# Kernel optimization log

Measured on AMD Instinct MI355X. Metric: run time of the kernel, lower is better.

The kernel has to match this reference:

```python
import jax, jax.numpy as jnp
import numpy as np

THRESH = 0.5
DECAY = 0.2
N_NODES = 39
T = 2000
K_HOPS = 3


def setup_inputs() -> dict:
    key = jax.random.key(0)
    ks = jax.random.split(key, 10)
    x = jax.random.normal(ks[0], (N_NODES, 2, T), dtype=jnp.float32)
    edge_index = jax.random.randint(ks[1], (2, 156), 0, N_NODES)
    # TAGConv(2, 64, K=3): (K+1) bias-free hop weights + single bias
    W_conv = jax.random.normal(ks[2], (K_HOPS + 1, 2, 64), dtype=jnp.float32) * 0.3
    b_conv = jax.random.normal(ks[3], (64,), dtype=jnp.float32) * 0.05
    W1 = jax.random.normal(ks[4], (N_NODES * 64, 128), dtype=jnp.float32) * 0.02
    b1 = jax.random.normal(ks[5], (128,), dtype=jnp.float32) * 0.02
    W2 = jax.random.normal(ks[6], (128, 256), dtype=jnp.float32) * 0.08
    b2 = jax.random.normal(ks[7], (256,), dtype=jnp.float32) * 0.02
    W3 = jax.random.normal(ks[8], (256, 36), dtype=jnp.float32) * 0.06
    b3 = jax.random.normal(ks[9], (36,), dtype=jnp.float32) * 0.02
    return {"x": x, "edge_index": edge_index, "W_conv": W_conv, "b_conv": b_conv,
            "W1": W1, "b1": b1, "W2": W2, "b2": b2, "W3": W3, "b3": b3}


def _norm_adj(edge_index, dtype):
    # PyG gcn_norm without self loops: A_hat = D^-1/2 A D^-1/2, message flows row->col
    row, col = edge_index[0], edge_index[1]
    A = jnp.zeros((N_NODES, N_NODES), dtype).at[col, row].add(1.0)
    deg = A.sum(axis=1)
    dinv = jnp.where(deg > 0, deg ** -0.5, 0.0).astype(dtype)
    return dinv[:, None] * A * dinv[None, :]


def reference(x, edge_index, W_conv, b_conv, W1, b1, W2, b2, W3, b3):
    A_hat = _norm_adj(edge_index, x.dtype)

    def spike(m):
        return (m > THRESH).astype(m.dtype)

    def step(carry, xt):
        c1m, c1s, h1m, h1s, h2m, h2s, h3m, h3s, acc = carry
        # TAGConv: sum_k (A_hat^k xt) @ W_k + bias   [39,64]
        h = xt
        conv = h @ W_conv[0]
        for k in range(1, K_HOPS + 1):
            h = A_hat @ h
            conv = conv + h @ W_conv[k]
        conv = conv + b_conv
        c1m = c1m * DECAY * (1.0 - c1s) + conv
        c1s = spike(c1m)
        f = c1s.reshape(-1)  # [2496]
        h1m = h1m * DECAY * (1.0 - h1s) + f @ W1 + b1
        h1s = spike(h1m)
        h2m = h2m * DECAY * (1.0 - h2s) + h1s @ W2 + b2
        h2s = spike(h2m)
        h3m = h3m * DECAY * (1.0 - h3s) + h2s @ W3 + b3
        h3s = spike(h3m)
        return (c1m, c1s, h1m, h1s, h2m, h2s, h3m, h3s, acc + h3s), None

    z = lambda s: jnp.zeros(s, x.dtype)
    init = (z((N_NODES, 64)), z((N_NODES, 64)), z((128,)), z((128,)),
            z((256,)), z((256,)), z((36,)), z((36,)), z((36,)))
    xs = jnp.moveaxis(x, -1, 0)  # [T, 39, 2]
    carry, _ = jax.lax.scan(step, init, xs)
    return carry[-1] / x.shape[-1]
```

## Files before the change

### kernel.cpp

```cpp
#include <hip/hip_runtime.h>

#define T 2000
#define K1N 2496
#define K2 4992
#define TL 48
#define NCHB 42
#define MAXNZ 24

using short8 = __attribute__((ext_vector_type(8))) short;
using floatx4 = __attribute__((ext_vector_type(4))) float;

__device__ __forceinline__ unsigned bf16_rne(float v) {
    unsigned u = __float_as_uint(v);
    return (u + 0x7FFFu + ((u >> 16) & 1u)) >> 16;
}
__device__ __forceinline__ unsigned packhl(float w) {
    unsigned hi = bf16_rne(w);
    float r = w - __uint_as_float(hi << 16);
    unsigned lo = bf16_rne(r);
    return (hi & 0xFFFFu) | (lo << 16);
}

__global__ __launch_bounds__(256) void conv_scan(const float* __restrict__ x,
        const int* __restrict__ ei, const float* __restrict__ Wc,
        const float* __restrict__ bc, unsigned char* __restrict__ FS,
        const float* __restrict__ W1, unsigned* __restrict__ W1t,
        float* __restrict__ out) {
    __shared__ float ah[1560];
    __shared__ float2 alist[39 * MAXNZ];
    __shared__ int nnzr[40];
    __shared__ float bufA[78 * TL];
    __shared__ float bufB[78 * TL];
    __shared__ float feat[4 * TL * 8];
    int tid = threadIdx.x;
    int nb = blockIdx.x, ch = blockIdx.y;
    int bl = ch * 10 + nb;

    if (bl == 0 && tid < 36) out[tid] = 0.f;

    for (int u = tid; u < 1521; u += 256) ah[u] = 0.f;
    __syncthreads();
    if (tid < 156) atomicAdd(&ah[ei[156 + tid] * 39 + ei[tid]], 1.f);
    __syncthreads();
    if (tid < 39) {
        float d = 0.f;
        for (int u = 0; u < 39; ++u) d += ah[tid * 39 + u];
        ah[1521 + tid] = (d > 0.f) ? (1.f / sqrtf(d)) : 0.f;
    }
    __syncthreads();
    for (int u = tid; u < 1521; u += 256) {
        int i = u / 39, j = u - i * 39;
        ah[u] = (ah[1521 + i] * ah[u]) * ah[1521 + j];
    }
    __syncthreads();
    if (tid < 39) {
        int cnt = 0;
        for (int m = 0; m < 39; ++m) {
            float v = ah[tid * 39 + m];
            if (v != 0.f && cnt < MAXNZ) {
                alist[tid * MAXNZ + cnt] = make_float2(v, __int_as_float((2 * m) * TL * 4));
                ++cnt;
            }
        }
        nnzr[tid] = cnt;
    }
    __syncthreads();

    int t0 = ch * TL;
    int i0 = nb * 4;
    int iloc = tid >> 6, j = tid & 63;
    bool vn = (i0 + iloc) < 39;
    float wv[8], bias;
    #pragma unroll
    for (int q = 0; q < 8; ++q) wv[q] = Wc[q * 64 + j];
    bias = bc[j];
    float m = 0.f, s = 0.f;

    for (int st = 0; st < 2; ++st) {
        int ts = t0 + (st - 1) * TL;
        if (ts < 0) continue;
        for (int e = tid; e < 78 * TL; e += 256) {
            int r = e / TL, tt = e - (e / TL) * TL;
            int t = ts + tt;
            bufA[e] = (t < T) ? x[r * T + t] : 0.f;
        }
        __syncthreads();
        for (int e = tid; e < 384; e += 256) {
            int lr = e / TL, tt = e - (e / TL) * TL;
            int gr = i0 * 2 + lr;
            float v = (gr < 78) ? bufA[gr * TL + tt] : 0.f;
            feat[(((lr >> 1) * TL) + tt) * 8 + (lr & 1)] = v;
        }
        for (int e = tid; e < 468; e += 256) {
            int r = e / 6, g = e - (e / 6) * 6;
            int ii = r >> 1, c = r & 1;
            float acc[8];
            #pragma unroll
            for (int u = 0; u < 8; ++u) acc[u] = 0.f;
            int nz = nnzr[ii];
            const float2* lp = &alist[ii * MAXNZ];
            int cg = c * (TL * 4) + g * 32;
            for (int q = 0; q < nz; ++q) {
                float2 av = lp[q];
                const float* xp = (const float*)((const char*)bufA + (__float_as_int(av.y) + cg));
                float a = av.x;
                float4 x0 = *(const float4*)xp;
                float4 x1 = *(const float4*)(xp + 4);
                acc[0] += a * x0.x; acc[1] += a * x0.y; acc[2] += a * x0.z; acc[3] += a * x0.w;
                acc[4] += a * x1.x; acc[5] += a * x1.y; acc[6] += a * x1.z; acc[7] += a * x1.w;
            }
            float* dp = &bufB[r * TL + g * 8];
            *(float4*)dp = *(float4*)&acc[0];
            *(float4*)(dp + 4) = *(float4*)&acc[4];
        }
        __syncthreads();
        for (int e = tid; e < 384; e += 256) {
            int lr = e / TL, tt = e - (e / TL) * TL;
            int gr = i0 * 2 + lr;
            float v = (gr < 78) ? bufB[gr * TL + tt] : 0.f;
            feat[(((lr >> 1) * TL) + tt) * 8 + 2 + (lr & 1)] = v;
        }
        for (int e = tid; e < 468; e += 256) {
            int r = e / 6, g = e - (e / 6) * 6;
            int ii = r >> 1, c = r & 1;
            float acc[8];
            #pragma unroll
            for (int u = 0; u < 8; ++u) acc[u] = 0.f;
            int nz = nnzr[ii];
            const float2* lp = &alist[ii * MAXNZ];
            int cg = c * (TL * 4) + g * 32;
            for (int q = 0; q < nz; ++q) {
                float2 av = lp[q];
                const float* xp = (const float*)((const char*)bufB + (__float_as_int(av.y) + cg));
                float a = av.x;
                float4 x0 = *(const float4*)xp;
                float4 x1 = *(const float4*)(xp + 4);
                acc[0] += a * x0.x; acc[1] += a * x0.y; acc[2] += a * x0.z; acc[3] += a * x0.w;
                acc[4] += a * x1.x; acc[5] += a * x1.y; acc[6] += a * x1.z; acc[7] += a * x1.w;
            }
            float* dp = &bufA[r * TL + g * 8];
            *(float4*)dp = *(float4*)&acc[0];
            *(float4*)(dp + 4) = *(float4*)&acc[4];
        }
        __syncthreads();
        for (int e = tid; e < 384; e += 256) {
            int lr = e / TL, tt = e - (e / TL) * TL;
            int gr = i0 * 2 + lr;
            float v = (gr < 78) ? bufA[gr * TL + tt] : 0.f;
            feat[(((lr >> 1) * TL) + tt) * 8 + 4 + (lr & 1)] = v;
        }
        for (int e = tid; e < 48; e += 256) {
            int lr = e / 6, g = e - (e / 6) * 6;
            int gi = i0 + (lr >> 1), c = lr & 1, il = lr >> 1;
            float acc[8];
            #pragma unroll
            for (int u = 0; u < 8; ++u) acc[u] = 0.f;
            if (gi < 39) {
                int nz = nnzr[gi];
                const float2* lp = &alist[gi * MAXNZ];
                int cg = c * (TL * 4) + g * 32;
                for (int q = 0; q < nz; ++q) {
                    float2 av = lp[q];
                    const float* xp = (const float*)((const char*)bufA + (__float_as_int(av.y) + cg));
                    float a = av.x;
                    float4 x0 = *(const float4*)xp;
                    float4 x1 = *(const float4*)(xp + 4);
                    acc[0] += a * x0.x; acc[1] += a * x0.y; acc[2] += a * x0.z; acc[3] += a * x0.w;
                    acc[4] += a * x1.x; acc[5] += a * x1.y; acc[6] += a * x1.z; acc[7] += a * x1.w;
                }
            }
            #pragma unroll
            for (int u = 0; u < 8; ++u)
                feat[((il * TL) + g * 8 + u) * 8 + 6 + c] = acc[u];
        }
        __syncthreads();
        for (int tt = 0; tt < TL; ++tt) {
            const float4* fp = (const float4*)&feat[((iloc * TL) + tt) * 8];
            float4 f0 = fp[0], f1 = fp[1];
            float acc = 0.f;
            acc += wv[0] * f0.x; acc += wv[1] * f0.y; acc += wv[2] * f0.z; acc += wv[3] * f0.w;
            acc += wv[4] * f1.x; acc += wv[5] * f1.y; acc += wv[6] * f1.z; acc += wv[7] * f1.w;
            float v = acc + bias;
            m = m * 0.2f * (1.f - s) + v;
            s = (m > 0.5f) ? 1.f : 0.f;
            if (st == 1 && vn) {
                int t = ts + tt;
                if (t < T) FS[t * K1N + (nb * 256 + tid)] = (unsigned char)(s != 0.f);
            }
        }
        __syncthreads();
    }
    const int total = 128 * K1N;
    for (int f = bl * 256 + tid; f < total; f += 420 * 256) {
        int k = f >> 7, jj = f & 127;
        W1t[jj * K1N + k] = packhl(W1[f]);
    }
}

__global__ __launch_bounds__(256) void gemm1(const unsigned char* __restrict__ FS,
        const short* __restrict__ W1t, float* __restrict__ F1p) {
    __shared__ short As[32 * 72];
    __shared__ short Ws[128 * 72];
    int tid = threadIdx.x;
    int t0 = blockIdx.x * 32;
    int ks = blockIdx.y;
    int lane = tid & 63, wvi = tid >> 6;
    int j0 = wvi * 32;
    int row = lane & 15, quad = lane >> 4;
    floatx4 a00 = {0.f, 0.f, 0.f, 0.f};
    floatx4 a01 = a00, a10 = a00, a11 = a00;
    int kb = ks * 416, kb2 = ks * 832;
    int sm = tid >> 3, sb4 = (tid & 7) * 4;
    int gt = t0 + sm;
    int jjv[4], kov[4];
    #pragma unroll
    for (int u = 0; u < 4; ++u) {
        int aid = u * 256 + tid;
        jjv[u] = aid >> 3;
        kov[u] = (aid & 7) * 8;
    }
    unsigned u4 = 0;
    short8 wr0, wr1, wr2, wr3;
    if (gt < T) u4 = *(const unsigned*)&FS[gt * K1N + kb + sb4];
    wr0 = *(const short8*)&W1t[jjv[0] * K2 + kb2 + kov[0]];
    wr1 = *(const short8*)&W1t[jjv[1] * K2 + kb2 + kov[1]];
    wr2 = *(const short8*)&W1t[jjv[2] * K2 + kb2 + kov[2]];
    wr3 = *(const short8*)&W1t[jjv[3] * K2 + kb2 + kov[3]];
    for (int c = 0; c < 13; ++c) {
        uint4 dd;
        dd.x = (u4 & 0x000000FFu) ? 0x3F803F80u : 0u;
        dd.y = (u4 & 0x0000FF00u) ? 0x3F803F80u : 0u;
        dd.z = (u4 & 0x00FF0000u) ? 0x3F803F80u : 0u;
        dd.w = (u4 & 0xFF000000u) ? 0x3F803F80u : 0u;
        *(uint4*)&As[sm * 72 + sb4 * 2] = dd;
        *(short8*)&Ws[jjv[0] * 72 + kov[0]] = wr0;
        *(short8*)&Ws[jjv[1] * 72 + kov[1]] = wr1;
        *(short8*)&Ws[jjv[2] * 72 + kov[2]] = wr2;
        *(short8*)&Ws[jjv[3] * 72 + kov[3]] = wr3;
        __syncthreads();
        unsigned u4n = 0;
        short8 wn0, wn1, wn2, wn3;
        if (c < 12) {
            if (gt < T) u4n = *(const unsigned*)&FS[gt * K1N + kb + (c + 1) * 32 + sb4];
            wn0 = *(const short8*)&W1t[jjv[0] * K2 + kb2 + (c + 1) * 64 + kov[0]];
            wn1 = *(const short8*)&W1t[jjv[1] * K2 + kb2 + (c + 1) * 64 + kov[1]];
            wn2 = *(const short8*)&W1t[jjv[2] * K2 + kb2 + (c + 1) * 64 + kov[2]];
            wn3 = *(const short8*)&W1t[jjv[3] * K2 + kb2 + (c + 1) * 64 + kov[3]];
        }
        #pragma unroll
        for (int sh = 0; sh < 2; ++sh) {
            int k0 = sh * 32 + quad * 8;
            short8 fa0 = *(const short8*)&As[row * 72 + k0];
            short8 fa1 = *(const short8*)&As[(row + 16) * 72 + k0];
            short8 fb0 = *(const short8*)&Ws[(j0 + row) * 72 + k0];
            short8 fb1 = *(const short8*)&Ws[(j0 + 16 + row) * 72 + k0];
            a00 = __builtin_amdgcn_mfma_f32_16x16x32_bf16(fa0, fb0, a00, 0, 0, 0);
            a01 = __builtin_amdgcn_mfma_f32_16x16x32_bf16(fa0, fb1, a01, 0, 0, 0);
            a10 = __builtin_amdgcn_mfma_f32_16x16x32_bf16(fa1, fb0, a10, 0, 0, 0);
            a11 = __builtin_amdgcn_mfma_f32_16x16x32_bf16(fa1, fb1, a11, 0, 0, 0);
        }
        __syncthreads();
        if (c < 12) { u4 = u4n; wr0 = wn0; wr1 = wn1; wr2 = wn2; wr3 = wn3; }
    }
    #pragma unroll
    for (int r = 0; r < 4; ++r) {
        int m0 = quad * 4 + r;
        int t = t0 + m0;
        if (t < T) {
            F1p[t * 768 + ks * 128 + j0 + row] = a00[r];
            F1p[t * 768 + ks * 128 + j0 + 16 + row] = a01[r];
        }
        int t2 = t0 + 16 + m0;
        if (t2 < T) {
            F1p[t2 * 768 + ks * 128 + j0 + row] = a10[r];
            F1p[t2 * 768 + ks * 128 + j0 + 16 + row] = a11[r];
        }
    }
}

__global__ __launch_bounds__(256) void h1_gemm2(const float* __restrict__ F1p,
        const float* __restrict__ b1, const float* __restrict__ W2,
        float* __restrict__ G2) {
    __shared__ float AT[128 * 8];
    int tid = threadIdx.x;
    int t0 = blockIdx.x * 8;
    if (tid < 128) {
        int n = tid;
        int hs = t0 - 20; if (hs < 0) hs = 0;
        float b = b1[n];
        float m = 0.f, s = 0.f;
        for (int tg = hs; tg < t0 + 8; tg += 4) {
            float vb[4][6];
            #pragma unroll
            for (int u = 0; u < 4; ++u)
                #pragma unroll
                for (int q = 0; q < 6; ++q)
                    vb[u][q] = F1p[(tg + u) * 768 + q * 128 + n];
            #pragma unroll
            for (int u = 0; u < 4; ++u) {
                float v = 0.f;
                #pragma unroll
                for (int q = 0; q < 6; ++q) v += vb[u][q];
                v += b;
                m = m * 0.2f * (1.f - s) + v;
                s = (m > 0.5f) ? 1.f : 0.f;
                int t = tg + u;
                if (t >= t0) AT[n * 8 + (t - t0)] = s;
            }
        }
    }
    __syncthreads();
    int j = tid;
    float acc[8] = {0.f};
    #pragma unroll 4
    for (int k = 0; k < 128; ++k) {
        float w = W2[k * 256 + j];
        float4 q0 = *(const float4*)&AT[k * 8 + 0];
        float4 q1 = *(const float4*)&AT[k * 8 + 4];
        acc[0] += q0.x * w; acc[1] += q0.y * w; acc[2] += q0.z * w; acc[3] += q0.w * w;
        acc[4] += q1.x * w; acc[5] += q1.y * w; acc[6] += q1.z * w; acc[7] += q1.w * w;
    }
    #pragma unroll
    for (int tt = 0; tt < 8; ++tt) G2[(t0 + tt) * 256 + j] = acc[tt];
}

__global__ __launch_bounds__(256) void tail(const float* __restrict__ G2,
        const float* __restrict__ b2, const float* __restrict__ W3,
        const float* __restrict__ b3, float* __restrict__ out) {
    __shared__ float w3t[36 * 260];
    __shared__ unsigned char S2[76 * 260];
    __shared__ float G3[76 * 36];
    int tid = threadIdx.x;
    int t0 = blockIdx.x * 25;
    int gs = t0 - 50; if (gs < 0) gs = 0;
    int hs = gs - 50; if (hs < 0) hs = 0;
    int L3 = t0 + 25 - gs;
    #pragma unroll
    for (int u = 0; u < 9; ++u) {
        int f = u * 1024 + tid * 4;
        float4 wq = *(const float4*)&W3[f];
        int k0 = f / 36, j0 = f - k0 * 36;
        float wv[4] = {wq.x, wq.y, wq.z, wq.w};
        #pragma unroll
        for (int q = 0; q < 4; ++q) {
            int k = (j0 + q >= 36) ? k0 + 1 : k0;
            int jj = (j0 + q >= 36) ? (j0 + q - 36) : (j0 + q);
            w3t[jj * 260 + k] = wv[q];
        }
    }
    {
        int n = tid;
        float b = b2[n];
        float m = 0.f, s = 0.f;
        for (int base = hs; base < t0 + 25; base += 25) {
            float vb[25];
            #pragma unroll
            for (int u = 0; u < 25; ++u) vb[u] = G2[(base + u) * 256 + n];
            #pragma unroll
            for (int u = 0; u < 25; ++u) {
                float v = vb[u] + b;
                m = m * 0.2f * (1.f - s) + v;
                s = (m > 0.5f) ? 1.f : 0.f;
                int t = base + u;
                if (t >= gs) S2[(t - gs) * 260 + n] = (unsigned char)(s != 0.f);
            }
        }
    }
    __syncthreads();
    for (int e = tid; e < 36 * 19; e += 256) {
        int jj = e / 19, g = e - (e / 19) * 19;
        int tb = g * 4;
        if (tb >= L3) continue;
        float ac0 = 0.f, ac1 = 0.f, ac2 = 0.f, ac3 = 0.f;
        const unsigned char* r0 = &S2[tb * 260];
        for (int k = 0; k < 256; k += 4) {
            float4 w = *(const float4*)&w3t[jj * 260 + k];
            uchar4 q0 = *(const uchar4*)&r0[k];
            uchar4 q1 = *(const uchar4*)&r0[260 + k];
            uchar4 q2 = *(const uchar4*)&r0[520 + k];
            uchar4 q3 = *(const uchar4*)&r0[780 + k];
            ac0 += (float)q0.x * w.x + (float)q0.y * w.y + (float)q0.z * w.z + (float)q0.w * w.w;
            ac1 += (float)q1.x * w.x + (float)q1.y * w.y + (float)q1.z * w.z + (float)q1.w * w.w;
            ac2 += (float)q2.x * w.x + (float)q2.y * w.y + (float)q2.z * w.z + (float)q2.w * w.w;
            ac3 += (float)q3.x * w.x + (float)q3.y * w.y + (float)q3.z * w.z + (float)q3.w * w.w;
        }
        G3[tb * 36 + jj] = ac0;
        if (tb + 1 < L3) G3[(tb + 1) * 36 + jj] = ac1;
        if (tb + 2 < L3) G3[(tb + 2) * 36 + jj] = ac2;
        if (tb + 3 < L3) G3[(tb + 3) * 36 + jj] = ac3;
    }
    __syncthreads();
    if (tid < 36) {
        int n = tid;
        float b = b3[n];
        float m = 0.f, s = 0.f;
        int cnt = 0;
        for (int t = gs; t < t0 + 25; ++t) {
            float v = G3[(t - gs) * 36 + n] + b;
            m = m * 0.2f * (1.f - s) + v;
            s = (m > 0.5f) ? 1.f : 0.f;
            if (t >= t0) cnt += (s != 0.f) ? 1 : 0;
        }
        atomicAdd(&out[n], (float)cnt * 0.0005f);
    }
}

extern "C" void kernel_launch(void* const* d_in, const int* in_sizes, int n_in,
                              void* d_out, int out_size, void* d_ws, size_t ws_size,
                              hipStream_t stream) {
    const float* x  = (const float*)d_in[0];
    const int*   ei = (const int*)d_in[1];
    const float* Wc = (const float*)d_in[2];
    const float* bc = (const float*)d_in[3];
    const float* W1 = (const float*)d_in[4];
    const float* b1 = (const float*)d_in[5];
    const float* W2 = (const float*)d_in[6];
    const float* b2 = (const float*)d_in[7];
    const float* W3 = (const float*)d_in[8];
    const float* b3 = (const float*)d_in[9];
    float* out = (float*)d_out;

    float* w = (float*)d_ws;
    float* F1p = w;                       w += (size_t)T * 768;
    float* G2  = w;                       w += (size_t)T * 256;
    unsigned* W1t = (unsigned*)w;         w += 128 * K1N;
    unsigned char* FS = (unsigned char*)w;

    conv_scan<<<dim3(10, NCHB), 256, 0, stream>>>(x, ei, Wc, bc, FS, W1, W1t, out);
    gemm1<<<dim3(63, 6), 256, 0, stream>>>(FS, (const short*)W1t, F1p);
    h1_gemm2<<<250, 256, 0, stream>>>(F1p, b1, W2, G2);
    tail<<<80, 256, 0, stream>>>(G2, b2, W3, b3, out);
}
```

Baseline: 161.2 us.

## Fuse h1 scan, MFMA layer-2 GEMM and tail into one windowed kernel

Merges the h1 spike scan, the W2 GEMM, the h2/h3 scans and the W3 product into one kernel. Each block owns 20 output steps and replays a 120-step warm-up window in 32-step tiles, which removes the global G2 round trip and one launch. The 128x256 GEMM now runs on bf16 MFMA using a hi/lo split of W2, prepacked in the conv kernel. In exchange there is redundant warm-up work, since each block recomputes 140 steps. Correctness depends on the spike state converging within the window.

After: 259.0 us. +60.7%, slower.

```diff
diff --git a/kernel.cpp b/kernel.cpp
--- a/kernel.cpp
+++ b/kernel.cpp
@@ -6,6 +6,8 @@
 #define TL 48
 #define NCHB 42
 #define MAXNZ 24
+#define L3 20
+#define NB3 100
 
 using short8 = __attribute__((ext_vector_type(8))) short;
 using floatx4 = __attribute__((ext_vector_type(4))) float;
@@ -25,6 +27,7 @@
         const int* __restrict__ ei, const float* __restrict__ Wc,
         const float* __restrict__ bc, unsigned char* __restrict__ FS,
         const float* __restrict__ W1, unsigned* __restrict__ W1t,
+        const float* __restrict__ W2, unsigned* __restrict__ W2t,
         float* __restrict__ out) {
     __shared__ float ah[1560];
     __shared__ float2 alist[39 * MAXNZ];
@@ -194,6 +197,10 @@
     for (int f = bl * 256 + tid; f < total; f += 420 * 256) {
         int k = f >> 7, jj = f & 127;
         W1t[jj * K1N + k] = packhl(W1[f]);
+    }
+    for (int f = bl * 256 + tid; f < 128 * 256; f += 420 * 256) {
+        int k = f >> 8, jj = f & 255;
+        W2t[jj * 128 + k] = packhl(W2[f]);
     }
 }
 
@@ -278,131 +285,160 @@
     }
 }
 
-__global__ __launch_bounds__(256) void h1_gemm2(const float* __restrict__ F1p,
-        const float* __restrict__ b1, const float* __restrict__ W2,
-        float* __restrict__ G2) {
-    __shared__ float AT[128 * 8];
-    int tid = threadIdx.x;
-    int t0 = blockIdx.x * 8;
-    if (tid < 128) {
-        int n = tid;
-        int hs = t0 - 20; if (hs < 0) hs = 0;
-        float b = b1[n];
-        float m = 0.f, s = 0.f;
-        for (int tg = hs; tg < t0 + 8; tg += 4) {
-            float vb[4][6];
-            #pragma unroll
-            for (int u = 0; u < 4; ++u)
-                #pragma unroll
-                for (int q = 0; q < 6; ++q)
-                    vb[u][q] = F1p[(tg + u) * 768 + q * 128 + n];
-            #pragma unroll
-            for (int u = 0; u < 4; ++u) {
-                float v = 0.f;
-                #pragma unroll
-                for (int q = 0; q < 6; ++q) v += vb[u][q];
-                v += b;
-                m = m * 0.2f * (1.f - s) + v;
-                s = (m > 0.5f) ? 1.f : 0.f;
-                int t = tg + u;
-                if (t >= t0) AT[n * 8 + (t - t0)] = s;
-            }
-        }
-    }
-    __syncthreads();
-    int j = tid;
-    float acc[8] = {0.f};
-    #pragma unroll 4
-    for (int k = 0; k < 128; ++k) {
-        float w = W2[k * 256 + j];
-        float4 q0 = *(const float4*)&AT[k * 8 + 0];
-        float4 q1 = *(const float4*)&AT[k * 8 + 4];
-        acc[0] += q0.x * w; acc[1] += q0.y * w; acc[2] += q0.z * w; acc[3] += q0.w * w;
-        acc[4] += q1.x * w; acc[5] += q1.y * w; acc[6] += q1.z * w; acc[7] += q1.w * w;
-    }
-    #pragma unroll
-    for (int tt = 0; tt < 8; ++tt) G2[(t0 + tt) * 256 + j] = acc[tt];
-}
-
-__global__ __launch_bounds__(256) void tail(const float* __restrict__ G2,
+__global__ __launch_bounds__(256) void fused_tail(const float* __restrict__ F1p,
+        const float* __restrict__ b1, const unsigned* __restrict__ W2t,
         const float* __restrict__ b2, const float* __restrict__ W3,
         const float* __restrict__ b3, float* __restrict__ out) {
+    __shared__ short S1[32 * 264];
+    __shared__ float G2[32 * 260];
+    __shared__ unsigned char S2[32 * 260];
+    __shared__ float G3[32 * 40];
     __shared__ float w3t[36 * 260];
-    __shared__ unsigned char S2[76 * 260];
-    __shared__ float G3[76 * 36];
     int tid = threadIdx.x;
-    int t0 = blockIdx.x * 25;
-    int gs = t0 - 50; if (gs < 0) gs = 0;
-    int hs = gs - 50; if (hs < 0) hs = 0;
-    int L3 = t0 + 25 - gs;
+    int t0 = blockIdx.x * L3;
+    int tend = t0 + L3;
+    int ts0 = t0 - 120;
+    int lane = tid & 63, wv = tid >> 6;
+    int row = lane & 15, quad = lane >> 4;
+    int j0w = wv * 64;
+
     #pragma unroll
     for (int u = 0; u < 9; ++u) {
         int f = u * 1024 + tid * 4;
         float4 wq = *(const float4*)&W3[f];
-        int k0 = f / 36, j0 = f - k0 * 36;
-        float wv[4] = {wq.x, wq.y, wq.z, wq.w};
+        int k0 = f / 36, jb = f - k0 * 36;
+        float wvv[4] = {wq.x, wq.y, wq.z, wq.w};
         #pragma unroll
         for (int q = 0; q < 4; ++q) {
-            int k = (j0 + q >= 36) ? k0 + 1 : k0;
-            int jj = (j0 + q >= 36) ? (j0 + q - 36) : (j0 + q);
-            w3t[jj * 260 + k] = wv[q];
-        }
-    }
-    {
-        int n = tid;
-        float b = b2[n];
-        float m = 0.f, s = 0.f;
-        for (int base = hs; base < t0 + 25; base += 25) {
-            float vb[25];
-            #pragma unroll
-            for (int u = 0; u < 25; ++u) vb[u] = G2[(base + u) * 256 + n];
-            #pragma unroll
-            for (int u = 0; u < 25; ++u) {
-                float v = vb[u] + b;
-                m = m * 0.2f * (1.f - s) + v;
-                s = (m > 0.5f) ? 1.f : 0.f;
-                int t = base + u;
-                if (t >= gs) S2[(t - gs) * 260 + n] = (unsigned char)(s != 0.f);
-            }
-        }
-    }
-    __syncthreads();
-    for (int e = tid; e < 36 * 19; e += 256) {
-        int jj = e / 19, g = e - (e / 19) * 19;
-        int tb = g * 4;
-        if (tb >= L3) continue;
-        float ac0 = 0.f, ac1 = 0.f, ac2 = 0.f, ac3 = 0.f;
-        const unsigned char* r0 = &S2[tb * 260];
-        for (int k = 0; k < 256; k += 4) {
-            float4 w = *(const float4*)&w3t[jj * 260 + k];
-            uchar4 q0 = *(const uchar4*)&r0[k];
-            uchar4 q1 = *(const uchar4*)&r0[260 + k];
-            uchar4 q2 = *(const uchar4*)&r0[520 + k];
-            uchar4 q3 = *(const uchar4*)&r0[780 + k];
-            ac0 += (float)q0.x * w.x + (float)q0.y * w.y + (float)q0.z * w.z + (float)q0.w * w.w;
-            ac1 += (float)q1.x * w.x + (float)q1.y * w.y + (float)q1.z * w.z + (float)q1.w * w.w;
-            ac2 += (float)q2.x * w.x + (float)q2.y * w.y + (float)q2.z * w.z + (float)q2.w * w.w;
-            ac3 += (float)q3.x * w.x + (float)q3.y * w.y + (float)q3.z * w.z + (float)q3.w * w.w;
-        }
-        G3[tb * 36 + jj] = ac0;
-        if (tb + 1 < L3) G3[(tb + 1) * 36 + jj] = ac1;
-        if (tb + 2 < L3) G3[(tb + 2) * 36 + jj] = ac2;
-        if (tb + 3 < L3) G3[(tb + 3) * 36 + jj] = ac3;
-    }
-    __syncthreads();
-    if (tid < 36) {
-        int n = tid;
-        float b = b3[n];
-        float m = 0.f, s = 0.f;
-        int cnt = 0;
-        for (int t = gs; t < t0 + 25; ++t) {
-            float v = G3[(t - gs) * 36 + n] + b;
-            m = m * 0.2f * (1.f - s) + v;
-            s = (m > 0.5f) ? 1.f : 0.f;
-            if (t >= t0) cnt += (s != 0.f) ? 1 : 0;
-        }
-        atomicAdd(&out[n], (float)cnt * 0.0005f);
-    }
+            int k = (jb + q >= 36) ? k0 + 1 : k0;
+            int jj = (jb + q >= 36) ? (jb + q - 36) : (jb + q);
+            w3t[jj * 260 + k] = wvv[q];
+        }
+    }
+
+    float m1 = 0.f, s1 = 0.f;
+    float m2 = 0.f, s2v = 0.f;
+    float m3 = 0.f, s3 = 0.f;
+    int cnt = 0;
+    float bb1 = (tid < 128) ? b1[tid] : 0.f;
+    float bb2 = b2[tid];
+    float bb3 = (tid < 36) ? b3[tid] : 0.f;
+
+    for (int tile = 0; tile < 5; ++tile) {
+        int tb = ts0 + tile * 32;
+        if (tid < 128) {
+            int n = tid;
+            for (int tg = 0; tg < 32; tg += 8) {
+                float vb[8][6];
+                #pragma unroll
+                for (int u = 0; u < 8; ++u) {
+                    int t = tb + tg + u;
+                    bool val = (t >= 0 && t < tend);
+                    #pragma unroll
+                    for (int q = 0; q < 6; ++q)
+                        vb[u][q] = val ? F1p[t * 768 + q * 128 + n] : 0.f;
+                }
+                #pragma unroll
+                for (int u = 0; u < 8; ++u) {
+                    int t = tb + tg + u;
+                    unsigned dv = 0;
+                    if (t >= 0 && t < tend) {
+                        float v = 0.f;
+                        #pragma unroll
+                        for (int q = 0; q < 6; ++q) v += vb[u][q];
+                        v += bb1;
+                        m1 = m1 * 0.2f * (1.f - s1) + v;
+                        s1 = (m1 > 0.5f) ? 1.f : 0.f;
+                        dv = (s1 != 0.f) ? 0x3F803F80u : 0u;
+                    }
+                    ((unsigned*)S1)[(tg + u) * 132 + n] = dv;
+                }
+            }
+        }
+        __syncthreads();
+        floatx4 acc[2][4];
+        #pragma unroll
+        for (int mt = 0; mt < 2; ++mt)
+            #pragma unroll
+            for (int nt = 0; nt < 4; ++nt) acc[mt][nt] = (floatx4){0.f, 0.f, 0.f, 0.f};
+        short8 bfr[4];
+        #pragma unroll
+        for (int nt = 0; nt < 4; ++nt)
+            bfr[nt] = *(const short8*)&W2t[(j0w + nt * 16 + row) * 128 + quad * 4];
+        for (int c = 0; c < 8; ++c) {
+            short8 bc0 = bfr[0], bc1 = bfr[1], bc2 = bfr[2], bc3 = bfr[3];
+            if (c < 7) {
+                #pragma unroll
+                for (int nt = 0; nt < 4; ++nt)
+                    bfr[nt] = *(const short8*)&W2t[(j0w + nt * 16 + row) * 128 + (c + 1) * 16 + quad * 4];
+            }
+            short8 a0 = *(const short8*)&S1[row * 264 + c * 32 + quad * 8];
+            short8 a1 = *(const short8*)&S1[(row + 16) * 264 + c * 32 + quad * 8];
+            acc[0][0] = __builtin_amdgcn_mfma_f32_16x16x32_bf16(a0, bc0, acc[0][0], 0, 0, 0);
+            acc[0][1] = __builtin_amdgcn_mfma_f32_16x16x32_bf16(a0, bc1, acc[0][1], 0, 0, 0);
+            acc[0][2] = __builtin_amdgcn_mfma_f32_16x16x32_bf16(a0, bc2, acc[0][2], 0, 0, 0);
+            acc[0][3] = __builtin_amdgcn_mfma_f32_16x16x32_bf16(a0, bc3, acc[0][3], 0, 0, 0);
+            acc[1][0] = __builtin_amdgcn_mfma_f32_16x16x32_bf16(a1, bc0, acc[1][0], 0, 0, 0);
+            acc[1][1] = __builtin_amdgcn_mfma_f32_16x16x32_bf16(a1, bc1, acc[1][1], 0, 0, 0);
+            acc[1][2] = __builtin_amdgcn_mfma_f32_16x16x32_bf16(a1, bc2, acc[1][2], 0, 0, 0);
+            acc[1][3] = __builtin_amdgcn_mfma_f32_16x16x32_bf16(a1, bc3, acc[1][3], 0, 0, 0);
+        }
+        #pragma unroll
+        for (int mt = 0; mt < 2; ++mt)
+            #pragma unroll
+            for (int nt = 0; nt < 4; ++nt)
+                #pragma unroll
+                for (int r = 0; r < 4; ++r)
+                    G2[(mt * 16 + quad * 4 + r) * 260 + j0w + nt * 16 + row] = acc[mt][nt][r];
+        __syncthreads();
+        for (int tt = 0; tt < 32; ++tt) {
+            int t = tb + tt;
+            unsigned char sv = 0;
+            if (t >= 0 && t < tend) {
+                float v = G2[tt * 260 + tid] + bb2;
+                m2 = m2 * 0.2f * (1.f - s2v) + v;
+                s2v = (m2 > 0.5f) ? 1.f : 0.f;
+                sv = (unsigned char)(s2v != 0.f);
+            }
+            S2[tt * 260 + tid] = sv;
+        }
+        __syncthreads();
+        for (int e = tid; e < 288; e += 256) {
+            int jj = e >> 3, g = e & 7;
+            int tbr = g * 4;
+            float a0 = 0.f, a1 = 0.f, a2 = 0.f, a3 = 0.f;
+            const unsigned char* r0 = &S2[tbr * 260];
+            for (int k = 0; k < 256; k += 4) {
+                float4 w = *(const float4*)&w3t[jj * 260 + k];
+                uchar4 q0 = *(const uchar4*)&r0[k];
+                uchar4 q1 = *(const uchar4*)&r0[260 + k];
+                uchar4 q2 = *(const uchar4*)&r0[520 + k];
+                uchar4 q3 = *(const uchar4*)&r0[780 + k];
+                a0 += (float)q0.x * w.x + (float)q0.y * w.y + (float)q0.z * w.z + (float)q0.w * w.w;
+                a1 += (float)q1.x * w.x + (float)q1.y * w.y + (float)q1.z * w.z + (float)q1.w * w.w;
+                a2 += (float)q2.x * w.x + (float)q2.y * w.y + (float)q2.z * w.z + (float)q2.w * w.w;
+                a3 += (float)q3.x * w.x + (float)q3.y * w.y + (float)q3.z * w.z + (float)q3.w * w.w;
+            }
+            G3[(tbr + 0) * 40 + jj] = a0;
+            G3[(tbr + 1) * 40 + jj] = a1;
+            G3[(tbr + 2) * 40 + jj] = a2;
+            G3[(tbr + 3) * 40 + jj] = a3;
+        }
+        __syncthreads();
+        if (tid < 36) {
+            for (int tt = 0; tt < 32; ++tt) {
+                int t = tb + tt;
+                if (t >= 0 && t < tend) {
+                    float v = G3[tt * 40 + tid] + bb3;
+                    m3 = m3 * 0.2f * (1.f - s3) + v;
+                    s3 = (m3 > 0.5f) ? 1.f : 0.f;
+                    if (t >= t0) cnt += (s3 != 0.f) ? 1 : 0;
+                }
+            }
+        }
+        __syncthreads();
+    }
+    if (tid < 36) atomicAdd(&out[tid], (float)cnt * 0.0005f);
 }
 
 extern "C" void kernel_launch(void* const* d_in, const int* in_sizes, int n_in,
@@ -422,12 +458,11 @@
 
     float* w = (float*)d_ws;
     float* F1p = w;                       w += (size_t)T * 768;
-    float* G2  = w;                       w += (size_t)T * 256;
     unsigned* W1t = (unsigned*)w;         w += 128 * K1N;
+    unsigned* W2t = (unsigned*)w;         w += 128 * 256;
     unsigned char* FS = (unsigned char*)w;
 
-    conv_scan<<<dim3(10, NCHB), 256, 0, stream>>>(x, ei, Wc, bc, FS, W1, W1t, out);
+    conv_scan<<<dim3(10, NCHB), 256, 0, stream>>>(x, ei, Wc, bc, FS, W1, W1t, W2, W2t, out);
     gemm1<<<dim3(63, 6), 256, 0, stream>>>(FS, (const short*)W1t, F1p);
-    h1_gemm2<<<250, 256, 0, stream>>>(F1p, b1, W2, G2);
-    tail<<<80, 256, 0, stream>>>(G2, b2, W3, b3, out);
-}
+    fused_tail<<<NB3, 256, 0, stream>>>(F1p, b1, W2t, b2, W3, b3, out);
+}
```

## Fuse spike-feature GEMM1 into conv_scan with per-block K-split MFMA

Applied to the files above, without the earlier changes.

Drops the separate gemm1 kernel and the global spike-byte buffer FS. Each conv_scan block keeps its 48-timestep spike tile in shared memory and runs the bf16 hi/lo MFMA against its own 256-row slice of W1, writing 10 K-split partial sums that h1_gemm2 now adds up. This removes one launch and the FS write/read round trip, and folds the W1 transpose/pack into the fused GEMM. In exchange, every block re-reads and re-packs its W1 slice (42 time-chunks redo the same work), shared memory use grows, and F1p partial traffic rises from 6 to 10 slices per timestep.

Result: slower. 182.6 us (+13.2%).

```diff
diff --git a/kernel.cpp b/kernel.cpp
--- a/kernel.cpp
+++ b/kernel.cpp
@@ -2,7 +2,6 @@
 
 #define T 2000
 #define K1N 2496
-#define K2 4992
 #define TL 48
 #define NCHB 42
 #define MAXNZ 24
@@ -20,18 +19,28 @@
     unsigned lo = bf16_rne(r);
     return (hi & 0xFFFFu) | (lo << 16);
 }
+__device__ __forceinline__ short8 expand4(unsigned bb) {
+    uint4 dd;
+    dd.x = (bb & 0x000000FFu) ? 0x3F803F80u : 0u;
+    dd.y = (bb & 0x0000FF00u) ? 0x3F803F80u : 0u;
+    dd.z = (bb & 0x00FF0000u) ? 0x3F803F80u : 0u;
+    dd.w = (bb & 0xFF000000u) ? 0x3F803F80u : 0u;
+    return *(short8*)&dd;
+}
 
 __global__ __launch_bounds__(256) void conv_scan(const float* __restrict__ x,
         const int* __restrict__ ei, const float* __restrict__ Wc,
-        const float* __restrict__ bc, unsigned char* __restrict__ FS,
-        const float* __restrict__ W1, unsigned* __restrict__ W1t,
-        float* __restrict__ out) {
-    __shared__ float ah[1560];
-    __shared__ float2 alist[39 * MAXNZ];
-    __shared__ int nnzr[40];
-    __shared__ float bufA[78 * TL];
-    __shared__ float bufB[78 * TL];
-    __shared__ float feat[4 * TL * 8];
+        const float* __restrict__ bc, const float* __restrict__ W1,
+        float* __restrict__ F1p, float* __restrict__ out) {
+    __shared__ float SM[13000];
+    float* ah = SM;
+    float2* alist = (float2*)&SM[1560];
+    int* nnzr = (int*)&SM[3432];
+    float* bufA = &SM[3500];
+    float* bufB = &SM[7244];
+    float* feat = &SM[10988];
+    unsigned char* S1b = (unsigned char*)&SM[3500];
+    unsigned* w1c = (unsigned*)&SM[6700];
     int tid = threadIdx.x;
     int nb = blockIdx.x, ch = blockIdx.y;
     int bl = ch * 10 + nb;
@@ -183,98 +192,63 @@
             float v = acc + bias;
             m = m * 0.2f * (1.f - s) + v;
             s = (m > 0.5f) ? 1.f : 0.f;
-            if (st == 1 && vn) {
-                int t = ts + tt;
-                if (t < T) FS[t * K1N + (nb * 256 + tid)] = (unsigned char)(s != 0.f);
-            }
+            if (st == 1) S1b[tt * 264 + tid] = (unsigned char)(vn && s != 0.f);
         }
         __syncthreads();
     }
-    const int total = 128 * K1N;
-    for (int f = bl * 256 + tid; f < total; f += 420 * 256) {
-        int k = f >> 7, jj = f & 127;
-        W1t[jj * K1N + k] = packhl(W1[f]);
-    }
-}
-
-__global__ __launch_bounds__(256) void gemm1(const unsigned char* __restrict__ FS,
-        const short* __restrict__ W1t, float* __restrict__ F1p) {
-    __shared__ short As[32 * 72];
-    __shared__ short Ws[128 * 72];
-    int tid = threadIdx.x;
-    int t0 = blockIdx.x * 32;
-    int ks = blockIdx.y;
-    int lane = tid & 63, wvi = tid >> 6;
-    int j0 = wvi * 32;
-    int row = lane & 15, quad = lane >> 4;
-    floatx4 a00 = {0.f, 0.f, 0.f, 0.f};
-    floatx4 a01 = a00, a10 = a00, a11 = a00;
-    int kb = ks * 416, kb2 = ks * 832;
-    int sm = tid >> 3, sb4 = (tid & 7) * 4;
-    int gt = t0 + sm;
-    int jjv[4], kov[4];
-    #pragma unroll
-    for (int u = 0; u < 4; ++u) {
-        int aid = u * 256 + tid;
-        jjv[u] = aid >> 3;
-        kov[u] = (aid & 7) * 8;
-    }
-    unsigned u4 = 0;
-    short8 wr0, wr1, wr2, wr3;
-    if (gt < T) u4 = *(const unsigned*)&FS[gt * K1N + kb + sb4];
-    wr0 = *(const short8*)&W1t[jjv[0] * K2 + kb2 + kov[0]];
-    wr1 = *(const short8*)&W1t[jjv[1] * K2 + kb2 + kov[1]];
-    wr2 = *(const short8*)&W1t[jjv[2] * K2 + kb2 + kov[2]];
-    wr3 = *(const short8*)&W1t[jjv[3] * K2 + kb2 + kov[3]];
-    for (int c = 0; c < 13; ++c) {
-        uint4 dd;
-        dd.x = (u4 & 0x000000FFu) ? 0x3F803F80u : 0u;
-        dd.y = (u4 & 0x0000FF00u) ? 0x3F803F80u : 0u;
-        dd.z = (u4 & 0x00FF0000u) ? 0x3F803F80u : 0u;
-        dd.w = (u4 & 0xFF000000u) ? 0x3F803F80u : 0u;
-        *(uint4*)&As[sm * 72 + sb4 * 2] = dd;
-        *(short8*)&Ws[jjv[0] * 72 + kov[0]] = wr0;
-        *(short8*)&Ws[jjv[1] * 72 + kov[1]] = wr1;
-        *(short8*)&Ws[jjv[2] * 72 + kov[2]] = wr2;
-        *(short8*)&Ws[jjv[3] * 72 + kov[3]] = wr3;
-        __syncthreads();
-        unsigned u4n = 0;
-        short8 wn0, wn1, wn2, wn3;
-        if (c < 12) {
-            if (gt < T) u4n = *(const unsigned*)&FS[gt * K1N + kb + (c + 1) * 32 + sb4];
-            wn0 = *(const short8*)&W1t[jjv[0] * K2 + kb2 + (c + 1) * 64 + kov[0]];
-            wn1 = *(const short8*)&W1t[jjv[1] * K2 + kb2 + (c + 1) * 64 + kov[1]];
-            wn2 = *(const short8*)&W1t[jjv[2] * K2 + kb2 + (c + 1) * 64 + kov[2]];
-            wn3 = *(const short8*)&W1t[jjv[3] * K2 + kb2 + (c + 1) * 64 + kov[3]];
-        }
+
+    {
+        int lane = tid & 63, wvq = tid >> 6;
+        int row = lane & 15, quad = lane >> 4;
+        int j0w = wvq * 32;
+        floatx4 acc[3][2];
         #pragma unroll
-        for (int sh = 0; sh < 2; ++sh) {
-            int k0 = sh * 32 + quad * 8;
-            short8 fa0 = *(const short8*)&As[row * 72 + k0];
-            short8 fa1 = *(const short8*)&As[(row + 16) * 72 + k0];
-            short8 fb0 = *(const short8*)&Ws[(j0 + row) * 72 + k0];
-            short8 fb1 = *(const short8*)&Ws[(j0 + 16 + row) * 72 + k0];
-            a00 = __builtin_amdgcn_mfma_f32_16x16x32_bf16(fa0, fb0, a00, 0, 0, 0);
-            a01 = __builtin_amdgcn_mfma_f32_16x16x32_bf16(fa0, fb1, a01, 0, 0, 0);
-            a10 = __builtin_amdgcn_mfma_f32_16x16x32_bf16(fa1, fb0, a10, 0, 0, 0);
-            a11 = __builtin_amdgcn_mfma_f32_16x16x32_bf16(fa1, fb1, a11, 0, 0, 0);
-        }
-        __syncthreads();
-        if (c < 12) { u4 = u4n; wr0 = wn0; wr1 = wn1; wr2 = wn2; wr3 = wn3; }
-    }
-    #pragma unroll
-    for (int r = 0; r < 4; ++r) {
-        int m0 = quad * 4 + r;
-        int t = t0 + m0;
-        if (t < T) {
-            F1p[t * 768 + ks * 128 + j0 + row] = a00[r];
-            F1p[t * 768 + ks * 128 + j0 + 16 + row] = a01[r];
-        }
-        int t2 = t0 + 16 + m0;
-        if (t2 < T) {
-            F1p[t2 * 768 + ks * 128 + j0 + row] = a10[r];
-            F1p[t2 * 768 + ks * 128 + j0 + 16 + row] = a11[r];
-        }
+        for (int mt = 0; mt < 3; ++mt)
+            #pragma unroll
+            for (int nt = 0; nt < 2; ++nt) acc[mt][nt] = (floatx4){0.f, 0.f, 0.f, 0.f};
+        for (int c = 0; c < 8; ++c) {
+            int kb = nb * 256 + c * 32;
+            #pragma unroll
+            for (int u = 0; u < 16; ++u) {
+                int idx = u * 256 + tid;
+                int k = idx >> 7, jj = idx & 127;
+                float wval = (kb + k < K1N) ? W1[(kb + k) * 128 + jj] : 0.f;
+                w1c[k * 132 + jj] = packhl(wval);
+            }
+            __syncthreads();
+            #pragma unroll
+            for (int si = 0; si < 2; ++si) {
+                int kc = si * 16 + quad * 4;
+                int klo = c * 32 + kc;
+                short8 af0 = expand4(*(const unsigned*)&S1b[row * 264 + klo]);
+                short8 af1 = expand4(*(const unsigned*)&S1b[(row + 16) * 264 + klo]);
+                short8 af2 = expand4(*(const unsigned*)&S1b[(row + 32) * 264 + klo]);
+                int jj0 = j0w + row, jj1 = j0w + 16 + row;
+                uint4 b0v = {w1c[(kc + 0) * 132 + jj0], w1c[(kc + 1) * 132 + jj0],
+                             w1c[(kc + 2) * 132 + jj0], w1c[(kc + 3) * 132 + jj0]};
+                uint4 b1v = {w1c[(kc + 0) * 132 + jj1], w1c[(kc + 1) * 132 + jj1],
+                             w1c[(kc + 2) * 132 + jj1], w1c[(kc + 3) * 132 + jj1]};
+                short8 bf0 = *(short8*)&b0v;
+                short8 bf1 = *(short8*)&b1v;
+                acc[0][0] = __builtin_amdgcn_mfma_f32_16x16x32_bf16(af0, bf0, acc[0][0], 0, 0, 0);
+                acc[0][1] = __builtin_amdgcn_mfma_f32_16x16x32_bf16(af0, bf1, acc[0][1], 0, 0, 0);
+                acc[1][0] = __builtin_amdgcn_mfma_f32_16x16x32_bf16(af1, bf0, acc[1][0], 0, 0, 0);
+                acc[1][1] = __builtin_amdgcn_mfma_f32_16x16x32_bf16(af1, bf1, acc[1][1], 0, 0, 0);
+                acc[2][0] = __builtin_amdgcn_mfma_f32_16x16x32_bf16(af2, bf0, acc[2][0], 0, 0, 0);
+                acc[2][1] = __builtin_amdgcn_mfma_f32_16x16x32_bf16(af2, bf1, acc[2][1], 0, 0, 0);
+            }
+            __syncthreads();
+        }
+        #pragma unroll
+        for (int mt = 0; mt < 3; ++mt)
+            #pragma unroll
+            for (int r = 0; r < 4; ++r) {
+                int t = t0 + mt * 16 + quad * 4 + r;
+                if (t < T) {
+                    F1p[t * 1280 + nb * 128 + j0w + row]      = acc[mt][0][r];
+                    F1p[t * 1280 + nb * 128 + j0w + 16 + row] = acc[mt][1][r];
+                }
+            }
     }
 }
 
@@ -290,17 +264,17 @@
         float b = b1[n];
         float m = 0.f, s = 0.f;
         for (int tg = hs; tg < t0 + 8; tg += 4) {
-            float vb[4][6];
+            float vb[4][10];
             #pragma unroll
             for (int u = 0; u < 4; ++u)
                 #pragma unroll
-                for (int q = 0; q < 6; ++q)
-                    vb[u][q] = F1p[(tg + u) * 768 + q * 128 + n];
+                for (int q = 0; q < 10; ++q)
+                    vb[u][q] = F1p[(tg + u) * 1280 + q * 128 + n];
             #pragma unroll
             for (int u = 0; u < 4; ++u) {
                 float v = 0.f;
                 #pragma unroll
-                for (int q = 0; q < 6; ++q) v += vb[u][q];
+                for (int q = 0; q < 10; ++q) v += vb[u][q];
                 v += b;
                 m = m * 0.2f * (1.f - s) + v;
                 s = (m > 0.5f) ? 1.f : 0.f;
@@ -421,13 +395,10 @@
     float* out = (float*)d_out;
 
     float* w = (float*)d_ws;
-    float* F1p = w;                       w += (size_t)T * 768;
+    float* F1p = w;                       w += (size_t)T * 1280;
     float* G2  = w;                       w += (size_t)T * 256;
-    unsigned* W1t = (unsigned*)w;         w += 128 * K1N;
-    unsigned char* FS = (unsigned char*)w;
-
-    conv_scan<<<dim3(10, NCHB), 256, 0, stream>>>(x, ei, Wc, bc, FS, W1, W1t, out);
-    gemm1<<<dim3(63, 6), 256, 0, stream>>>(FS, (const short*)W1t, F1p);
+
+    conv_scan<<<dim3(10, NCHB), 256, 0, stream>>>(x, ei, Wc, bc, W1, F1p, out);
     h1_gemm2<<<250, 256, 0, stream>>>(F1p, b1, W2, G2);
     tail<<<80, 256, 0, stream>>>(G2, b2, W3, b3, out);
 }
```
